# Optimization experiments

Hardware: AMD Instinct MI355X
Metric: run time of the kernel (lower is better)

## Reference

```python
import jax, jax.numpy as jnp
import numpy as np

B, L, H = 32, 4096, 64
C_U, C_X, N_OUT = 3, 1, 1
NL = 4
MODES = [512, 1024, 2048]


def setup_inputs() -> dict:
    key = jax.random.key(0)
    ks = jax.random.split(key, 16)
    scale = 1.0 / H  # 1/sqrt(in_ch*out_ch) with in_ch=out_ch=H
    inp = {
        'u': jax.random.normal(ks[0], (B, C_U, L), dtype=jnp.float32),
        'x': jax.random.uniform(ks[1], (B, C_X, L), dtype=jnp.float32),
        'enc_w': jax.random.normal(ks[2], (H, C_U + C_X), dtype=jnp.float32) * 0.5,
        'enc_b': jax.random.normal(ks[3], (H,), dtype=jnp.float32) * 0.1,
        'dec_w': jax.random.normal(ks[4], (N_OUT, H), dtype=jnp.float32) * 0.125,
        'dec_b': jax.random.normal(ks[5], (N_OUT,), dtype=jnp.float32) * 0.1,
        'conv1_w': jax.random.normal(ks[6], (NL, H, H), dtype=jnp.float32) * 0.125,
        'conv1_b': jax.random.normal(ks[7], (NL, H), dtype=jnp.float32) * 0.1,
        'conv2_w': jax.random.normal(ks[8], (NL, H, H), dtype=jnp.float32) * 0.125,
        'conv2_b': jax.random.normal(ks[9], (NL, H), dtype=jnp.float32) * 0.1,
        'spec_w0': jax.random.normal(ks[10], (NL, H, H, MODES[0], 2), dtype=jnp.float32) * scale,
        'spec_b0': jax.random.normal(ks[11], (NL, H), dtype=jnp.float32) * 0.1,
        'spec_w1': jax.random.normal(ks[12], (NL, H, H, MODES[1], 2), dtype=jnp.float32) * scale,
        'spec_b1': jax.random.normal(ks[13], (NL, H), dtype=jnp.float32) * 0.1,
        'spec_w2': jax.random.normal(ks[14], (NL, H, H, MODES[2], 2), dtype=jnp.float32) * scale,
        'spec_b2': jax.random.normal(ks[15], (NL, H), dtype=jnp.float32) * 0.1,
    }
    return inp


def _conv1x1(w, b, v):
    # 1x1 Conv1d: (O,I) x (B,I,L) -> (B,O,L)
    return jnp.einsum('oi,bil->bol', w, v) + b[None, :, None]


def _spectral(v, w_ri, b, n):
    # w_ri: (I,O,m,2) real/imag; v: (B,I,L)
    w = w_ri[..., 0] + 1j * w_ri[..., 1]
    m = w.shape[-1]
    x_low = jnp.fft.rfft(v, axis=-1)[:, :, :m]          # (B,I,m) complex
    y_ft = jnp.einsum('bim,iom->bom', x_low, w)          # (B,O,m)
    y = jnp.fft.irfft(y_ft, n=n, axis=-1)                # (B,O,L) real
    return y + b[None, :, None]


def reference(u, x, enc_w, enc_b, dec_w, dec_b, conv1_w, conv1_b, conv2_w, conv2_b,
              spec_w0, spec_b0, spec_w1, spec_b1, spec_w2, spec_b2):
    v = jnp.concatenate([x, u], axis=1)                  # (B, C_X+C_U, L)
    v = _conv1x1(enc_w, enc_b, v)                        # (B, H, L)
    spec_ws = (spec_w0, spec_w1, spec_w2)
    spec_bs = (spec_b0, spec_b1, spec_b2)
    n = v.shape[-1]
    for l in range(NL):
        spec_sum = _spectral(v, spec_ws[0][l], spec_bs[0][l], n)
        for k in range(1, len(spec_ws)):
            spec_sum = spec_sum + _spectral(v, spec_ws[k][l], spec_bs[k][l], n)
        h = jax.nn.gelu(_conv1x1(conv1_w[l], conv1_b[l], spec_sum))
        v = v + _conv1x1(conv2_w[l], conv2_b[l], h)
    return _conv1x1(dec_w, dec_b, v)                     # (B, N_OUT, L)
```

## Files before the change

kernel.cpp:

```cpp
#include <hip/hip_runtime.h>
#include <math.h>

#ifndef M_PI
#define M_PI 3.14159265358979323846
#endif

#define LEN   4096
#define NB    32
#define NH    64
#define NF    2048
#define NLAYER 4

__device__ __forceinline__ float2 cmul(float2 a, float2 b) {
    return make_float2(a.x*b.x - a.y*b.y, a.x*b.y + a.y*b.x);
}

__device__ __forceinline__ void twpow16(float2 w1, float2 W[16]) {
    W[0] = make_float2(1.0f, 0.0f);
    W[1] = w1;
    W[2] = cmul(w1, w1);
    W[3] = cmul(W[2], W[1]);
    W[4] = cmul(W[2], W[2]);
    W[5] = cmul(W[4], W[1]);
    W[6] = cmul(W[4], W[2]);
    W[7] = cmul(W[4], W[3]);
    W[8] = cmul(W[4], W[4]);
    W[9]  = cmul(W[8], W[1]);
    W[10] = cmul(W[8], W[2]);
    W[11] = cmul(W[8], W[3]);
    W[12] = cmul(W[8], W[4]);
    W[13] = cmul(W[8], W[5]);
    W[14] = cmul(W[8], W[6]);
    W[15] = cmul(W[8], W[7]);
}

__device__ __forceinline__ void gll16(const void* g, void* l) {
    __builtin_amdgcn_global_load_lds(
        (const __attribute__((address_space(1))) void*)g,
        (__attribute__((address_space(3))) void*)l, 16, 0, 0);
}

__global__ __launch_bounds__(256) void fill_tw(float2* __restrict__ tw) {
    int k = blockIdx.x * 256 + threadIdx.x;
    if (k < 4096) {
        double ang = -2.0 * M_PI * (double)k / 4096.0;
        tw[k] = make_float2((float)cos(ang), (float)sin(ang));
    }
}

__global__ __launch_bounds__(256) void w2t_k(
        const float* __restrict__ w2, float* __restrict__ w2t) {
    int idx = blockIdx.x * 256 + threadIdx.x;
    int l = idx >> 12;
    int r = idx & 4095;
    int o = r >> 6, i = r & 63;
    w2t[l * 4096 + i * 64 + o] = w2[idx];
}

#define BR16_INIT const int BR[16] = {0,8,4,12,2,10,6,14,1,9,5,13,3,11,7,15}

template<bool INV>
__device__ __forceinline__ void fft16(float2 z[16]) {
    const float S  = INV ? 1.0f : -1.0f;
    const float C1 = 0.9238795325112867f, S1 = 0.3826834323650898f;
    const float C2 = 0.7071067811865476f;
    const float2 W16[8] = {{1.f,0.f},{C1,S*S1},{C2,S*C2},{S1,S*C1},
                           {0.f,S},{-S1,S*C1},{-C2,S*C2},{-C1,S*S1}};
    const float2 W8[4]  = {{1.f,0.f},{C2,S*C2},{0.f,S},{-C2,S*C2}};
    #pragma unroll
    for (int i = 0; i < 8; ++i) {
        float2 u = z[i], v = z[i+8];
        z[i]   = make_float2(u.x+v.x, u.y+v.y);
        float2 d = make_float2(u.x-v.x, u.y-v.y);
        z[i+8] = cmul(d, W16[i]);
    }
    #pragma unroll
    for (int h = 0; h < 16; h += 8)
        #pragma unroll
        for (int i = 0; i < 4; ++i) {
            float2 u = z[h+i], v = z[h+i+4];
            z[h+i]   = make_float2(u.x+v.x, u.y+v.y);
            float2 d = make_float2(u.x-v.x, u.y-v.y);
            z[h+i+4] = cmul(d, W8[i]);
        }
    #pragma unroll
    for (int h = 0; h < 16; h += 4) {
        { float2 u = z[h],   v = z[h+2];
          z[h]   = make_float2(u.x+v.x, u.y+v.y);
          z[h+2] = make_float2(u.x-v.x, u.y-v.y); }
        { float2 u = z[h+1], v = z[h+3];
          z[h+1] = make_float2(u.x+v.x, u.y+v.y);
          float2 d = make_float2(u.x-v.x, u.y-v.y);
          z[h+3] = make_float2(-S*d.y, S*d.x); }
    }
    #pragma unroll
    for (int h = 0; h < 16; h += 2) {
        float2 u = z[h], v = z[h+1];
        z[h]   = make_float2(u.x+v.x, u.y+v.y);
        z[h+1] = make_float2(u.x-v.x, u.y-v.y);
    }
}

__global__ __launch_bounds__(256) void encoder_k(
        const float* __restrict__ x, const float* __restrict__ u,
        const float* __restrict__ ew, const float* __restrict__ eb,
        float* __restrict__ v) {
    int tid = blockIdx.x * 256 + threadIdx.x;
    int b = tid >> 12;
    int l = tid & (LEN - 1);
    float xv = x[(size_t)b * LEN + l];
    float u0 = u[((size_t)b * 3 + 0) * LEN + l];
    float u1 = u[((size_t)b * 3 + 1) * LEN + l];
    float u2 = u[((size_t)b * 3 + 2) * LEN + l];
    for (int h = 0; h < NH; ++h) {
        float a = eb[h] + ew[h*4+0]*xv + ew[h*4+1]*u0 + ew[h*4+2]*u1 + ew[h*4+3]*u2;
        v[((size_t)b * NH + h) * LEN + l] = a;
    }
}

__global__ __launch_bounds__(256) void fft_fwd_k(
        const float* __restrict__ vin, float2* __restrict__ Xt,
        const float2* __restrict__ tw) {
    __shared__ float2 lds[4352];
    BR16_INIT;
    int p = blockIdx.x;
    const float* s1 = vin + (size_t)(2*p)   * LEN;
    const float* s2 = vin + (size_t)(2*p+1) * LEN;
    int t = threadIdx.x;
    float2 z[16];
    #pragma unroll
    for (int a = 0; a < 16; ++a)
        z[a] = make_float2(s1[a*256 + t], s2[a*256 + t]);
    fft16<false>(z);
    {
        float2 Wp[16];
        twpow16(tw[t], Wp);
        #pragma unroll
        for (int r = 0; r < 16; ++r) {
            int ka = BR[r];
            lds[ka*256 + t] = cmul(z[r], Wp[ka]);
        }
    }
    __syncthreads();
    int ka = t >> 4, bp = t & 15;
    #pragma unroll
    for (int a2 = 0; a2 < 16; ++a2)
        z[a2] = lds[ka*256 + a2*16 + bp];
    __syncthreads();
    fft16<false>(z);
    {
        float2 Wq[16];
        twpow16(tw[16*bp], Wq);
        #pragma unroll
        for (int r = 0; r < 16; ++r) {
            int kap = BR[r];
            lds[kap*272 + ka*17 + bp] = cmul(z[r], Wq[kap]);
        }
    }
    __syncthreads();
    int kap2 = t >> 4, ka2 = t & 15;
    #pragma unroll
    for (int b2 = 0; b2 < 16; ++b2)
        z[b2] = lds[kap2*272 + ka2*17 + b2];
    __syncthreads();
    fft16<false>(z);
    #pragma unroll
    for (int r = 0; r < 16; ++r)
        lds[t + 256*BR[r]] = z[r];
    __syncthreads();
    float2* d1 = Xt + (size_t)(2*p)   * NF;
    float2* d2 = Xt + (size_t)(2*p+1) * NF;
    for (int j = 0; j < 8; ++j) {
        int f = t + j * 256;
        float2 Zf = lds[f];
        float2 Zm = lds[(4096 - f) & 4095];
        d1[f] = make_float2(0.5f * (Zf.x + Zm.x), 0.5f * (Zf.y - Zm.y));
        d2[f] = make_float2(0.5f * (Zf.y + Zm.y), 0.5f * (Zm.x - Zf.x));
    }
}

__device__ __forceinline__ float2 load_partial(
        const float2* __restrict__ r2, const float2* __restrict__ r1,
        const float2* __restrict__ r0, int f) {
    float2 y = r2[f];
    if (f < 1024) {
        float2 q = r1[f]; y.x += q.x; y.y += q.y;
        if (f < 512) { float2 w = r0[f]; y.x += w.x; y.y += w.y; }
    }
    return y;
}

__global__ __launch_bounds__(256) void fft_inv_k(
        const float2* __restrict__ Y2, const float2* __restrict__ Y1,
        const float2* __restrict__ Y0, float* __restrict__ sout,
        const float2* __restrict__ tw,
        const float* __restrict__ sb0, const float* __restrict__ sb1,
        const float* __restrict__ sb2, int layer) {
    __shared__ float2 lds[4352];
    BR16_INIT;
    int p = blockIdx.x;
    int o = (2 * p) & (NH - 1);
    const float2* r1_2 = Y2 + (size_t)(2*p)   * 2048;
    const float2* r2_2 = Y2 + (size_t)(2*p+1) * 2048;
    const float2* r1_1 = Y1 + (size_t)(2*p)   * 1024;
    const float2* r2_1 = Y1 + (size_t)(2*p+1) * 1024;
    const float2* r1_0 = Y0 + (size_t)(2*p)   * 512;
    const float2* r2_0 = Y0 + (size_t)(2*p+1) * 512;
    int t = threadIdx.x;
    float2 z[16];
    #pragma unroll
    for (int a = 0; a < 16; ++a) {
        int f = a * 256 + t;
        float2 zf;
        if (f < 2048) {
            float2 y1 = load_partial(r1_2, r1_1, r1_0, f);
            float2 y2 = load_partial(r2_2, r2_1, r2_0, f);
            if (f == 0) zf = make_float2(y1.x, y2.x);
            else        zf = make_float2(y1.x - y2.y, y1.y + y2.x);
        } else if (f == 2048) {
            zf = make_float2(0.0f, 0.0f);
        } else {
            int m = 4096 - f;
            float2 y1 = load_partial(r1_2, r1_1, r1_0, m);
            float2 y2 = load_partial(r2_2, r2_1, r2_0, m);
            zf = make_float2(y1.x + y2.y, y2.x - y1.y);
        }
        z[a] = zf;
    }
    fft16<true>(z);
    {
        float2 w1 = tw[t]; w1.y = -w1.y;
        float2 Wp[16];
        twpow16(w1, Wp);
        #pragma unroll
        for (int r = 0; r < 16; ++r) {
            int ka = BR[r];
            lds[ka*256 + t] = cmul(z[r], Wp[ka]);
        }
    }
    __syncthreads();
    int ka = t >> 4, bp = t & 15;
    #pragma unroll
    for (int a2 = 0; a2 < 16; ++a2)
        z[a2] = lds[ka*256 + a2*16 + bp];
    __syncthreads();
    fft16<true>(z);
    {
        float2 w16 = tw[16*bp]; w16.y = -w16.y;
        float2 Wq[16];
        twpow16(w16, Wq);
        #pragma unroll
        for (int r = 0; r < 16; ++r) {
            int kap = BR[r];
            lds[kap*272 + ka*17 + bp] = cmul(z[r], Wq[kap]);
        }
    }
    __syncthreads();
    int kap2 = t >> 4, ka2 = t & 15;
    #pragma unroll
    for (int b2 = 0; b2 < 16; ++b2)
        z[b2] = lds[kap2*272 + ka2*17 + b2];
    fft16<true>(z);
    float bias1 = sb0[layer*NH+o]   + sb1[layer*NH+o]   + sb2[layer*NH+o];
    float bias2 = sb0[layer*NH+o+1] + sb1[layer*NH+o+1] + sb2[layer*NH+o+1];
    float* d1 = sout + (size_t)(2*p)   * LEN;
    float* d2 = sout + (size_t)(2*p+1) * LEN;
    const float sc = 1.0f / 4096.0f;
    #pragma unroll
    for (int r = 0; r < 16; ++r) {
        int l = t + 256 * BR[r];
        d1[l] = z[r].x * sc + bias1;
        d2[l] = z[r].y * sc + bias2;
    }
}

__global__ __launch_bounds__(256) void specmm_k(
        const float2* __restrict__ X,
        float2* __restrict__ Y2p, float2* __restrict__ Y1p, float2* __restrict__ Y0p,
        const float* __restrict__ w0, const float* __restrict__ w1,
        const float* __restrict__ w2, int layer) {
    __shared__ float2 Xb[3][1024];
    __shared__ float2 Wb[3][512];

    int n   = blockIdx.x;
    int xcd = n & 7;
    int s   = n >> 3;
    int k, ftile, og;
    if (s < 96) {
        int h = s / 12, sib = s - h * 12;
        ftile = xcd * 8 + h;
        og = sib & 3;  k = sib >> 2;
    } else if (s < 160) {
        int m = (s - 96) >> 3, sib = (s - 96) & 7;
        ftile = 64 + xcd * 8 + m;
        og = sib & 3;  k = 2 - (sib >> 2);
    } else {
        int l2 = (s - 160) >> 2, sib = (s - 160) & 3;
        ftile = 128 + xcd * 16 + l2;
        og = sib;      k = 2;
    }
    int f0 = ftile * 8;

    const float2* wbp; float2* Yb; size_t mk;
    if (k == 2)      { wbp = (const float2*)w2 + (size_t)layer*NH*NH*2048; Yb = Y2p; mk = 2048; }
    else if (k == 1) { wbp = (const float2*)w1 + (size_t)layer*NH*NH*1024; Yb = Y1p; mk = 1024; }
    else             { wbp = (const float2*)w0 + (size_t)layer*NH*NH*512;  Yb = Y0p; mk = 512;  }

    int t  = threadIdx.x;
    int ff = t & 7;
    int u  = t >> 3;
    int b0  = (u & 7) * 4;
    int oo0 = (u >> 3) * 4;

    const int wv = t >> 6;
    const int ln = t & 63;
    const int bs = ln >> 2;
    const int sl = ln & 3;

    float2 acc[4][4];
    #pragma unroll
    for (int bb = 0; bb < 4; ++bb)
        #pragma unroll
        for (int oo = 0; oo < 4; ++oo)
            acc[bb][oo] = make_float2(0.0f, 0.0f);

    const float2* gx0; const float2* gx1;
    {
        int b = bs;
        int fp = sl ^ ((b >> 2) & 3);
        gx0 = X + ((size_t)b * NH + wv) * 2048 + f0 + 2*fp;
        b = 16 + bs;
        fp = sl ^ ((b >> 2) & 3);
        gx1 = X + ((size_t)b * NH + wv) * 2048 + f0 + 2*fp;
    }
    const float2* gw = wbp + ((size_t)wv * NH + og*16 + bs) * mk + f0 + 2*sl;

    #define STAGE(ic_, nb_)                                                     \
    {                                                                           \
        gll16(gx0 + (size_t)(ic_)*4*2048, &Xb[nb_][(wv*32 +  0)*8]);            \
        gll16(gx1 + (size_t)(ic_)*4*2048, &Xb[nb_][(wv*32 + 16)*8]);            \
        gll16(gw  + (size_t)(ic_)*256*mk, &Wb[nb_][wv*128]);                    \
    }

    STAGE(0, 0);
    STAGE(1, 1);
    STAGE(2, 2);
    int cb = 0;
    for (int ic = 0; ic < 16; ++ic) {
        if (ic < 14)       asm volatile("s_waitcnt vmcnt(6)" ::: "memory");
        else if (ic == 14) asm volatile("s_waitcnt vmcnt(3)" ::: "memory");
        else               asm volatile("s_waitcnt vmcnt(0)" ::: "memory");
        __builtin_amdgcn_sched_barrier(0);
        __builtin_amdgcn_s_barrier();
        #pragma unroll
        for (int ii = 0; ii < 4; ++ii) {
            float2 xr[4], wr[4];
            #pragma unroll
            for (int bb = 0; bb < 4; ++bb) {
                int b = b0 + bb;
                int slot = (ff >> 1) ^ ((b >> 2) & 3);
                xr[bb] = Xb[cb][((ii*32 + b)*4 + slot)*2 + (ff & 1)];
            }
            #pragma unroll
            for (int oo = 0; oo < 4; ++oo)
                wr[oo] = Wb[cb][((ii*16 + oo0 + oo)*4 + (ff >> 1))*2 + (ff & 1)];
            #pragma unroll
            for (int bb = 0; bb < 4; ++bb)
                #pragma unroll
                for (int oo = 0; oo < 4; ++oo) {
                    acc[bb][oo].x += xr[bb].x * wr[oo].x - xr[bb].y * wr[oo].y;
                    acc[bb][oo].y += xr[bb].x * wr[oo].y + xr[bb].y * wr[oo].x;
                }
        }
        __builtin_amdgcn_s_barrier();
        if (ic < 13) STAGE(ic + 3, cb);
        cb = (cb == 2) ? 0 : cb + 1;
    }
    #undef STAGE

    #pragma unroll
    for (int bb = 0; bb < 4; ++bb)
        #pragma unroll
        for (int oo = 0; oo < 4; ++oo)
            Yb[((size_t)(b0 + bb) * NH + og * 16 + oo0 + oo) * mk + f0 + ff] = acc[bb][oo];
}

__global__ __launch_bounds__(256) void conv_fused_k(
        const float* __restrict__ s,
        const float* __restrict__ c1w, const float* __restrict__ c1b,
        const float* __restrict__ w2t, const float* __restrict__ c2b,
        int layer, float* __restrict__ v,
        const float* __restrict__ dw, const float* __restrict__ db,
        float* __restrict__ out, int last) {
    int tid = blockIdx.x * 256 + threadIdx.x;
    int b = tid >> 12;
    int l = tid & (LEN - 1);
    float xr[NH];
    #pragma unroll
    for (int i = 0; i < NH; ++i) xr[i] = s[((size_t)b * NH + i) * LEN + l];
    const float* w1 = c1w + (size_t)layer * NH * NH;
    const float* b1 = c1b + layer * NH;
    const float* w2 = w2t + (size_t)layer * NH * NH;
    const float* b2 = c2b + layer * NH;
    float acc2[NH];
    #pragma unroll
    for (int o = 0; o < NH; ++o) acc2[o] = b2[o];
    for (int i = 0; i < NH; ++i) {
        const float* wr = w1 + i * NH;
        float a0 = 0.0f, a1 = 0.0f, a2 = 0.0f, a3 = 0.0f;
        #pragma unroll
        for (int k = 0; k < NH; k += 4) {
            a0 += wr[k]     * xr[k];
            a1 += wr[k + 1] * xr[k + 1];
            a2 += wr[k + 2] * xr[k + 2];
            a3 += wr[k + 3] * xr[k + 3];
        }
        float acc = b1[i] + ((a0 + a1) + (a2 + a3));
        float cc = 0.7978845608028654f * (acc + 0.044715f * acc * acc * acc);
        float e  = __expf(2.0f * cc);
        float th = 1.0f - 2.0f / (e + 1.0f);
        float h  = 0.5f * acc * (1.0f + th);
        const float* wc = w2 + i * NH;
        #pragma unroll
        for (int o = 0; o < NH; ++o) acc2[o] += wc[o] * h;
    }
    if (!last) {
        #pragma unroll
        for (int o = 0; o < NH; ++o) {
            size_t idx = ((size_t)b * NH + o) * LEN + l;
            v[idx] = v[idx] + acc2[o];
        }
    } else {
        float acc = db[0];
        #pragma unroll
        for (int o = 0; o < NH; ++o) {
            size_t idx = ((size_t)b * NH + o) * LEN + l;
            acc += dw[o] * (v[idx] + acc2[o]);
        }
        out[(size_t)b * LEN + l] = acc;
    }
}

extern "C" void kernel_launch(void* const* d_in, const int* in_sizes, int n_in,
                              void* d_out, int out_size, void* d_ws, size_t ws_size,
                              hipStream_t stream) {
    const float* u_in   = (const float*)d_in[0];
    const float* x_in   = (const float*)d_in[1];
    const float* enc_w  = (const float*)d_in[2];
    const float* enc_b  = (const float*)d_in[3];
    const float* dec_w  = (const float*)d_in[4];
    const float* dec_b  = (const float*)d_in[5];
    const float* conv1w = (const float*)d_in[6];
    const float* conv1b = (const float*)d_in[7];
    const float* conv2w = (const float*)d_in[8];
    const float* conv2b = (const float*)d_in[9];
    const float* sw0    = (const float*)d_in[10];
    const float* sb0    = (const float*)d_in[11];
    const float* sw1    = (const float*)d_in[12];
    const float* sb1    = (const float*)d_in[13];
    const float* sw2    = (const float*)d_in[14];
    const float* sb2    = (const float*)d_in[15];

    const size_t CPLX = (size_t)2048 * 2048;
    const size_t REAL = (size_t)NB * NH * LEN;
    char* base = (char*)d_ws;
    float2* tw   = (float2*)base;
    float2* bufA = (float2*)(base + 32768);
    float2* Y2p  = bufA + CPLX;
    float2* Y1p  = Y2p + CPLX;
    float2* Y0p  = Y1p + (size_t)2048 * 1024;
    float*  sbuf = (float*)(Y0p + (size_t)2048 * 512);
    float*  vbuf = sbuf + REAL;
    float*  w2tb = vbuf + REAL;
    size_t need = 32768 + (CPLX + CPLX + (size_t)2048*1024 + (size_t)2048*512) * sizeof(float2)
                + 2 * REAL * sizeof(float) + (size_t)NLAYER*NH*NH*sizeof(float);
    if (ws_size < need) return;

    fill_tw<<<16, 256, 0, stream>>>(tw);
    w2t_k<<<64, 256, 0, stream>>>(conv2w, w2tb);
    encoder_k<<<(NB * LEN) / 256, 256, 0, stream>>>(x_in, u_in, enc_w, enc_b, vbuf);

    for (int l = 0; l < NLAYER; ++l) {
        fft_fwd_k  <<<NB * NH / 2, 256, 0, stream>>>(vbuf, bufA, tw);
        specmm_k   <<<1792, 256, 0, stream>>>(bufA, Y2p, Y1p, Y0p, sw0, sw1, sw2, l);
        fft_inv_k  <<<NB * NH / 2, 256, 0, stream>>>(Y2p, Y1p, Y0p, sbuf, tw,
                                                     sb0, sb1, sb2, l);
        conv_fused_k<<<(NB * LEN) / 256, 256, 0, stream>>>(sbuf, conv1w, conv1b,
                                                           w2tb, conv2b, l, vbuf,
                                                           dec_w, dec_b, (float*)d_out,
                                                           l == NLAYER - 1);
    }
}
```

Baseline: 1.149 ms.

## Sum spectral weights across mode sets before the complex matmul

The three spectral convolutions share the same input FFT, so the weights for overlapping low frequencies are summed (w0+w1+w2) while being loaded, and one complex matmul over all 2048 modes is done instead of three separate ones. This cuts specmm work from 3584 to 2048 frequency tiles, drops two partial output buffers, and removes the partial-sum gathering in the inverse FFT. In exchange the weight path moves from async global-to-LDS loads with a triple buffer to register loads plus a VALU add and an LDS store with double buffering. That may expose more load latency per tile.

```diff
diff --git a/kernel.cpp b/kernel.cpp
--- a/kernel.cpp
+++ b/kernel.cpp
@@ -179,20 +179,8 @@
     }
 }
 
-__device__ __forceinline__ float2 load_partial(
-        const float2* __restrict__ r2, const float2* __restrict__ r1,
-        const float2* __restrict__ r0, int f) {
-    float2 y = r2[f];
-    if (f < 1024) {
-        float2 q = r1[f]; y.x += q.x; y.y += q.y;
-        if (f < 512) { float2 w = r0[f]; y.x += w.x; y.y += w.y; }
-    }
-    return y;
-}
-
 __global__ __launch_bounds__(256) void fft_inv_k(
-        const float2* __restrict__ Y2, const float2* __restrict__ Y1,
-        const float2* __restrict__ Y0, float* __restrict__ sout,
+        const float2* __restrict__ Yt, float* __restrict__ sout,
         const float2* __restrict__ tw,
         const float* __restrict__ sb0, const float* __restrict__ sb1,
         const float* __restrict__ sb2, int layer) {
@@ -200,12 +188,8 @@
     BR16_INIT;
     int p = blockIdx.x;
     int o = (2 * p) & (NH - 1);
-    const float2* r1_2 = Y2 + (size_t)(2*p)   * 2048;
-    const float2* r2_2 = Y2 + (size_t)(2*p+1) * 2048;
-    const float2* r1_1 = Y1 + (size_t)(2*p)   * 1024;
-    const float2* r2_1 = Y1 + (size_t)(2*p+1) * 1024;
-    const float2* r1_0 = Y0 + (size_t)(2*p)   * 512;
-    const float2* r2_0 = Y0 + (size_t)(2*p+1) * 512;
+    const float2* s1 = Yt + (size_t)(2*p)   * NF;
+    const float2* s2 = Yt + (size_t)(2*p+1) * NF;
     int t = threadIdx.x;
     float2 z[16];
     #pragma unroll
@@ -213,16 +197,16 @@
         int f = a * 256 + t;
         float2 zf;
         if (f < 2048) {
-            float2 y1 = load_partial(r1_2, r1_1, r1_0, f);
-            float2 y2 = load_partial(r2_2, r2_1, r2_0, f);
+            float2 y1 = s1[f];
+            float2 y2 = s2[f];
             if (f == 0) zf = make_float2(y1.x, y2.x);
             else        zf = make_float2(y1.x - y2.y, y1.y + y2.x);
         } else if (f == 2048) {
             zf = make_float2(0.0f, 0.0f);
         } else {
             int m = 4096 - f;
-            float2 y1 = load_partial(r1_2, r1_1, r1_0, m);
-            float2 y2 = load_partial(r2_2, r2_1, r2_0, m);
+            float2 y1 = s1[m];
+            float2 y2 = s2[m];
             zf = make_float2(y1.x + y2.y, y2.x - y1.y);
         }
         z[a] = zf;
@@ -275,36 +259,25 @@
 }
 
 __global__ __launch_bounds__(256) void specmm_k(
-        const float2* __restrict__ X,
-        float2* __restrict__ Y2p, float2* __restrict__ Y1p, float2* __restrict__ Y0p,
+        const float2* __restrict__ X, float2* __restrict__ Y,
         const float* __restrict__ w0, const float* __restrict__ w1,
         const float* __restrict__ w2, int layer) {
-    __shared__ float2 Xb[3][1024];
-    __shared__ float2 Wb[3][512];
+    __shared__ float2 Xb[2][1024];
+    __shared__ float2 Wb[2][512];
 
     int n   = blockIdx.x;
     int xcd = n & 7;
     int s   = n >> 3;
-    int k, ftile, og;
-    if (s < 96) {
-        int h = s / 12, sib = s - h * 12;
-        ftile = xcd * 8 + h;
-        og = sib & 3;  k = sib >> 2;
-    } else if (s < 160) {
-        int m = (s - 96) >> 3, sib = (s - 96) & 7;
-        ftile = 64 + xcd * 8 + m;
-        og = sib & 3;  k = 2 - (sib >> 2);
-    } else {
-        int l2 = (s - 160) >> 2, sib = (s - 160) & 3;
-        ftile = 128 + xcd * 16 + l2;
-        og = sib;      k = 2;
-    }
+    int og  = s & 3;
+    int tl  = s >> 2;
+    int ftile = (tl & 3) * 64 + (tl >> 2) * 8 + xcd;
     int f0 = ftile * 8;
-
-    const float2* wbp; float2* Yb; size_t mk;
-    if (k == 2)      { wbp = (const float2*)w2 + (size_t)layer*NH*NH*2048; Yb = Y2p; mk = 2048; }
-    else if (k == 1) { wbp = (const float2*)w1 + (size_t)layer*NH*NH*1024; Yb = Y1p; mk = 1024; }
-    else             { wbp = (const float2*)w0 + (size_t)layer*NH*NH*512;  Yb = Y0p; mk = 512;  }
+    const bool has1 = (f0 < 1024);
+    const bool has0 = (f0 < 512);
+
+    const float2* w2b = (const float2*)w2 + (size_t)layer * NH * NH * 2048;
+    const float2* w1b = (const float2*)w1 + (size_t)layer * NH * NH * 1024;
+    const float2* w0b = (const float2*)w0 + (size_t)layer * NH * NH * 512;
 
     int t  = threadIdx.x;
     int ff = t & 7;
@@ -333,25 +306,42 @@
         fp = sl ^ ((b >> 2) & 3);
         gx1 = X + ((size_t)b * NH + wv) * 2048 + f0 + 2*fp;
     }
-    const float2* gw = wbp + ((size_t)wv * NH + og*16 + bs) * mk + f0 + 2*sl;
-
-    #define STAGE(ic_, nb_)                                                     \
+    const size_t io = (size_t)wv * NH + og * 16 + bs;
+    const float2* gw2 = w2b + io * 2048 + f0 + 2*sl;
+    const float2* gw1 = w1b + io * 1024 + f0 + 2*sl;
+    const float2* gw0 = w0b + io * 512  + f0 + 2*sl;
+
+    #define STAGE_X(ic_, nb_)                                                   \
     {                                                                           \
         gll16(gx0 + (size_t)(ic_)*4*2048, &Xb[nb_][(wv*32 +  0)*8]);            \
         gll16(gx1 + (size_t)(ic_)*4*2048, &Xb[nb_][(wv*32 + 16)*8]);            \
-        gll16(gw  + (size_t)(ic_)*256*mk, &Wb[nb_][wv*128]);                    \
-    }
-
-    STAGE(0, 0);
-    STAGE(1, 1);
-    STAGE(2, 2);
-    int cb = 0;
+    }
+    float2 l2a, l2b, l1a, l1b, l0a, l0b;
+    #define WISSUE(ic_)                                                         \
+    {                                                                           \
+        const float2* p2 = gw2 + (size_t)(ic_)*256*2048;                        \
+        l2a = p2[0]; l2b = p2[1];                                               \
+        if (has1) { const float2* p1 = gw1 + (size_t)(ic_)*256*1024;            \
+                    l1a = p1[0]; l1b = p1[1]; }                                 \
+        if (has0) { const float2* p0 = gw0 + (size_t)(ic_)*256*512;             \
+                    l0a = p0[0]; l0b = p0[1]; }                                 \
+    }
+    #define WSUM_STORE(nb_)                                                     \
+    {                                                                           \
+        float2 wa = l2a, wc = l2b;                                              \
+        if (has1) { wa.x += l1a.x; wa.y += l1a.y; wc.x += l1b.x; wc.y += l1b.y; } \
+        if (has0) { wa.x += l0a.x; wa.y += l0a.y; wc.x += l0b.x; wc.y += l0b.y; } \
+        Wb[nb_][wv*128 + ln*2]     = wa;                                        \
+        Wb[nb_][wv*128 + ln*2 + 1] = wc;                                        \
+    }
+
+    WISSUE(0);
+    STAGE_X(0, 0);
+    WSUM_STORE(0);
+    __syncthreads();
+    int buf = 0;
     for (int ic = 0; ic < 16; ++ic) {
-        if (ic < 14)       asm volatile("s_waitcnt vmcnt(6)" ::: "memory");
-        else if (ic == 14) asm volatile("s_waitcnt vmcnt(3)" ::: "memory");
-        else               asm volatile("s_waitcnt vmcnt(0)" ::: "memory");
-        __builtin_amdgcn_sched_barrier(0);
-        __builtin_amdgcn_s_barrier();
+        if (ic < 15) { STAGE_X(ic + 1, buf ^ 1); WISSUE(ic + 1); }
         #pragma unroll
         for (int ii = 0; ii < 4; ++ii) {
             float2 xr[4], wr[4];
@@ -359,11 +349,11 @@
             for (int bb = 0; bb < 4; ++bb) {
                 int b = b0 + bb;
                 int slot = (ff >> 1) ^ ((b >> 2) & 3);
-                xr[bb] = Xb[cb][((ii*32 + b)*4 + slot)*2 + (ff & 1)];
+                xr[bb] = Xb[buf][((ii*32 + b)*4 + slot)*2 + (ff & 1)];
             }
             #pragma unroll
             for (int oo = 0; oo < 4; ++oo)
-                wr[oo] = Wb[cb][((ii*16 + oo0 + oo)*4 + (ff >> 1))*2 + (ff & 1)];
+                wr[oo] = Wb[buf][((ii*16 + oo0 + oo)*4 + (ff >> 1))*2 + (ff & 1)];
             #pragma unroll
             for (int bb = 0; bb < 4; ++bb)
                 #pragma unroll
@@ -372,17 +362,19 @@
                     acc[bb][oo].y += xr[bb].x * wr[oo].y + xr[bb].y * wr[oo].x;
                 }
         }
-        __builtin_amdgcn_s_barrier();
-        if (ic < 13) STAGE(ic + 3, cb);
-        cb = (cb == 2) ? 0 : cb + 1;
-    }
-    #undef STAGE
+        if (ic < 15) WSUM_STORE(buf ^ 1);
+        __syncthreads();
+        buf ^= 1;
+    }
+    #undef STAGE_X
+    #undef WISSUE
+    #undef WSUM_STORE
 
     #pragma unroll
     for (int bb = 0; bb < 4; ++bb)
         #pragma unroll
         for (int oo = 0; oo < 4; ++oo)
-            Yb[((size_t)(b0 + bb) * NH + og * 16 + oo0 + oo) * mk + f0 + ff] = acc[bb][oo];
+            Y[((size_t)(b0 + bb) * NH + og * 16 + oo0 + oo) * 2048 + f0 + ff] = acc[bb][oo];
 }
 
 __global__ __launch_bounds__(256) void conv_fused_k(
@@ -466,14 +458,12 @@
     char* base = (char*)d_ws;
     float2* tw   = (float2*)base;
     float2* bufA = (float2*)(base + 32768);
-    float2* Y2p  = bufA + CPLX;
-    float2* Y1p  = Y2p + CPLX;
-    float2* Y0p  = Y1p + (size_t)2048 * 1024;
-    float*  sbuf = (float*)(Y0p + (size_t)2048 * 512);
+    float2* bufB = bufA + CPLX;
+    float*  sbuf = (float*)(bufB + CPLX);
     float*  vbuf = sbuf + REAL;
     float*  w2tb = vbuf + REAL;
-    size_t need = 32768 + (CPLX + CPLX + (size_t)2048*1024 + (size_t)2048*512) * sizeof(float2)
-                + 2 * REAL * sizeof(float) + (size_t)NLAYER*NH*NH*sizeof(float);
+    size_t need = 32768 + 2 * CPLX * sizeof(float2) + 2 * REAL * sizeof(float)
+                + (size_t)NLAYER * NH * NH * sizeof(float);
     if (ws_size < need) return;
 
     fill_tw<<<16, 256, 0, stream>>>(tw);
@@ -482,8 +472,8 @@
 
     for (int l = 0; l < NLAYER; ++l) {
         fft_fwd_k  <<<NB * NH / 2, 256, 0, stream>>>(vbuf, bufA, tw);
-        specmm_k   <<<1792, 256, 0, stream>>>(bufA, Y2p, Y1p, Y0p, sw0, sw1, sw2, l);
-        fft_inv_k  <<<NB * NH / 2, 256, 0, stream>>>(Y2p, Y1p, Y0p, sbuf, tw,
+        specmm_k   <<<1024, 256, 0, stream>>>(bufA, bufB, sw0, sw1, sw2, l);
+        fft_inv_k  <<<NB * NH / 2, 256, 0, stream>>>(bufB, sbuf, tw,
                                                      sb0, sb1, sb2, l);
         conv_fused_k<<<(NB * LEN) / 256, 256, 0, stream>>>(sbuf, conv1w, conv1b,
                                                            w2tb, conv2b, l, vbuf,
```

Result: no change. 1.149 ms (+0.0%).
